# Kernel optimization log

Hardware: AMD Instinct MI355X
Metric: run time of the kernel (lower is better)

The kernel has to match this reference:

```python
import jax, jax.numpy as jnp
import numpy as np

N_NODES = 100000   # batch of target nodes
K = 10             # sampled neighbors per node (num_sample default)
VOCAB = 200000     # total graph nodes in embedding table
D = 128            # embed_dim


def setup_inputs() -> dict:
    key = jax.random.key(0)
    k1, k2, k3 = jax.random.split(key, 3)
    embed_table = jax.random.normal(k1, (VOCAB, D), dtype=jnp.float32)
    attn_w = jax.random.normal(k2, (D,), dtype=jnp.float32)
    neigh_idx = jax.random.randint(k3, (N_NODES, K), 0, VOCAB, dtype=jnp.int64)
    return {"embed_table": embed_table, "attn_w": attn_w, "neigh_idx": neigh_idx}


def reference(embed_table, attn_w, neigh_idx):
    # Gather neighbor embeddings: [N, K, D] (the irregular-access hot spot)
    feats = embed_table[neigh_idx]
    # attention_fc: Linear(D, 1, bias=False) -> scores [N, K]
    scores = jnp.einsum("nkd,d->nk", feats, attn_w)
    # softmax over the neighbor axis (dim=0 in the per-node torch loop == K here)
    weights = jax.nn.softmax(scores, axis=1)
    # attention-weighted sum of neighbor features -> [N, D]
    out = jnp.einsum("nk,nkd->nd", weights, feats)
    return out
```

## Files before the change

### kernel.cpp

```cpp
#include <hip/hip_runtime.h>
#include <math.h>


#define KNEIGH 10
#define DIM 128

__global__ __launch_bounds__(256) void attn_agg_kernel(
    const float* __restrict__ table,
    const float* __restrict__ attn_w,
    const int*   __restrict__ idx,
    float*       __restrict__ out,
    int n_nodes)
{
    const int gtid = blockIdx.x * blockDim.x + threadIdx.x;
    const int node = gtid >> 6;
    const int lane = threadIdx.x & 63;
    if (node >= n_nodes) return;

    const float2 wv = *(const float2*)(attn_w + lane * 2);

    int my_idx = 0;
    if (lane < KNEIGH) my_idx = idx[node * KNEIGH + lane];

    float2 f[KNEIGH];
    float  s[KNEIGH];

    #pragma unroll
    for (int k = 0; k < KNEIGH; ++k) {
        const int id = __shfl(my_idx, k, 64);
        f[k] = *(const float2*)(table + (size_t)id * DIM + lane * 2);
        float p = f[k].x * wv.x + f[k].y * wv.y;
        #pragma unroll
        for (int off = 32; off >= 1; off >>= 1)
            p += __shfl_xor(p, off, 64);
        s[k] = p;
    }

    float m = s[0];
    #pragma unroll
    for (int k = 1; k < KNEIGH; ++k) m = fmaxf(m, s[k]);
    float denom = 0.f;
    #pragma unroll
    for (int k = 0; k < KNEIGH; ++k) { s[k] = __expf(s[k] - m); denom += s[k]; }
    const float inv = 1.0f / denom;

    float2 acc = make_float2(0.f, 0.f);
    #pragma unroll
    for (int k = 0; k < KNEIGH; ++k) {
        const float wk = s[k] * inv;
        acc.x = fmaf(wk, f[k].x, acc.x);
        acc.y = fmaf(wk, f[k].y, acc.y);
    }

    *(float2*)(out + (size_t)node * DIM + lane * 2) = acc;
}

extern "C" void kernel_launch(void* const* d_in, const int* in_sizes, int n_in,
                              void* d_out, int out_size, void* d_ws, size_t ws_size,
                              hipStream_t stream) {
    const float* table  = (const float*)d_in[0];
    const float* attn_w = (const float*)d_in[1];
    const int*   idx    = (const int*)d_in[2];
    float*       out    = (float*)d_out;

    const int n_nodes = in_sizes[2] / KNEIGH;
    const int waves_per_block = 4;
    const int blocks = (n_nodes + waves_per_block - 1) / waves_per_block;
    attn_agg_kernel<<<blocks, 256, 0, stream>>>(table, attn_w, idx, out, n_nodes);
}
```

Measured before the change: 209.5 us.

## Split wave into two halves each gathering alternate neighbors with float4 loads

Result: no change. 209.5 us (+0.0%).

```diff
diff --git a/kernel.cpp b/kernel.cpp
--- a/kernel.cpp
+++ b/kernel.cpp
@@ -3,7 +3,8 @@
 
 
 #define KNEIGH 10
-#define DIM 128
+#define NPAIR  5
+#define DIM    128
 
 __global__ __launch_bounds__(256) void attn_agg_kernel(
     const float* __restrict__ table,
@@ -14,26 +15,36 @@
 {
     const int gtid = blockIdx.x * blockDim.x + threadIdx.x;
     const int node = gtid >> 6;
+    if (node >= n_nodes) return;
     const int lane = threadIdx.x & 63;
-    if (node >= n_nodes) return;
+    const int half = lane >> 5;
+    const int sub  = lane & 31;
 
-    const float2 wv = *(const float2*)(attn_w + lane * 2);
+    const float4 w4 = *(const float4*)(attn_w + sub * 4);
 
     int my_idx = 0;
     if (lane < KNEIGH) my_idx = idx[node * KNEIGH + lane];
 
-    float2 f[KNEIGH];
-    float  s[KNEIGH];
+    int id[NPAIR];
+    #pragma unroll
+    for (int j = 0; j < NPAIR; ++j)
+        id[j] = __shfl(my_idx, 2 * j + half, 64);
 
+    float4 f[NPAIR];
     #pragma unroll
-    for (int k = 0; k < KNEIGH; ++k) {
-        const int id = __shfl(my_idx, k, 64);
-        f[k] = *(const float2*)(table + (size_t)id * DIM + lane * 2);
-        float p = f[k].x * wv.x + f[k].y * wv.y;
+    for (int j = 0; j < NPAIR; ++j)
+        f[j] = *(const float4*)(table + (size_t)id[j] * DIM + sub * 4);
+
+    float s[KNEIGH];
+    #pragma unroll
+    for (int j = 0; j < NPAIR; ++j) {
+        float p = f[j].x * w4.x + f[j].y * w4.y + f[j].z * w4.z + f[j].w * w4.w;
         #pragma unroll
-        for (int off = 32; off >= 1; off >>= 1)
+        for (int off = 16; off >= 1; off >>= 1)
             p += __shfl_xor(p, off, 64);
-        s[k] = p;
+        const float q = __shfl_xor(p, 32, 64);
+        s[2 * j]     = half ? q : p;
+        s[2 * j + 1] = half ? p : q;
     }
 
     float m = s[0];
@@ -44,15 +55,23 @@
     for (int k = 0; k < KNEIGH; ++k) { s[k] = __expf(s[k] - m); denom += s[k]; }
     const float inv = 1.0f / denom;
 
-    float2 acc = make_float2(0.f, 0.f);
+    float4 acc = make_float4(0.f, 0.f, 0.f, 0.f);
     #pragma unroll
-    for (int k = 0; k < KNEIGH; ++k) {
-        const float wk = s[k] * inv;
-        acc.x = fmaf(wk, f[k].x, acc.x);
-        acc.y = fmaf(wk, f[k].y, acc.y);
+    for (int j = 0; j < NPAIR; ++j) {
+        const float wk = (half ? s[2 * j + 1] : s[2 * j]) * inv;
+        acc.x = fmaf(wk, f[j].x, acc.x);
+        acc.y = fmaf(wk, f[j].y, acc.y);
+        acc.z = fmaf(wk, f[j].z, acc.z);
+        acc.w = fmaf(wk, f[j].w, acc.w);
     }
 
-    *(float2*)(out + (size_t)node * DIM + lane * 2) = acc;
+    acc.x += __shfl_xor(acc.x, 32, 64);
+    acc.y += __shfl_xor(acc.y, 32, 64);
+    acc.z += __shfl_xor(acc.z, 32, 64);
+    acc.w += __shfl_xor(acc.w, 32, 64);
+
+    if (half == 0)
+        *(float4*)(out + (size_t)node * DIM + sub * 4) = acc;
 }
 
 extern "C" void kernel_launch(void* const* d_in, const int* in_sizes, int n_in,
```

## Precompute per-row scores and bf16 table, then gather half-width rows

Applied to the files above, without the earlier changes.

New measurement: 219.7 us. 4.9% more time.

```diff
diff --git a/kernel.cpp b/kernel.cpp
--- a/kernel.cpp
+++ b/kernel.cpp
@@ -3,9 +3,114 @@
 
 
 #define KNEIGH 10
-#define DIM 128
+#define NPAIR  5
+#define DIM    128
 
-__global__ __launch_bounds__(256) void attn_agg_kernel(
+__global__ __launch_bounds__(256) void convert_score_kernel(
+    const float*  __restrict__ table,
+    const float*  __restrict__ attn_w,
+    unsigned int* __restrict__ bf_table,
+    float*        __restrict__ scores,
+    int vocab)
+{
+    const int gtid = blockIdx.x * blockDim.x + threadIdx.x;
+    const int row  = gtid >> 6;
+    if (row >= vocab) return;
+    const int lane = threadIdx.x & 63;
+
+    const float2 f = *(const float2*)(table  + (size_t)row * DIM + lane * 2);
+    const float2 w = *(const float2*)(attn_w + lane * 2);
+
+    float p = f.x * w.x + f.y * w.y;
+    #pragma unroll
+    for (int off = 32; off >= 1; off >>= 1)
+        p += __shfl_xor(p, off, 64);
+
+    unsigned int bx = __float_as_uint(f.x);
+    unsigned int by = __float_as_uint(f.y);
+    bx = (bx + 0x7fffu + ((bx >> 16) & 1u)) >> 16;
+    by = (by + 0x7fffu + ((by >> 16) & 1u)) & 0xffff0000u;
+    bf_table[(size_t)row * 64 + lane] = bx | by;
+
+    if (lane == 0) scores[row] = p;
+}
+
+__global__ __launch_bounds__(256) void attn_gather_kernel(
+    const unsigned int* __restrict__ bf_table,
+    const float*        __restrict__ scores,
+    const int*          __restrict__ idx,
+    float*              __restrict__ out,
+    int n_nodes)
+{
+    const int gtid = blockIdx.x * blockDim.x + threadIdx.x;
+    const int node = gtid >> 6;
+    if (node >= n_nodes) return;
+    const int lane = threadIdx.x & 63;
+    const int half = lane >> 5;
+    const int sub  = lane & 31;
+
+    const int base = __builtin_amdgcn_readfirstlane(node) * KNEIGH;
+    int id0 = idx[base + 0], id1 = idx[base + 1], id2 = idx[base + 2],
+        id3 = idx[base + 3], id4 = idx[base + 4], id5 = idx[base + 5],
+        id6 = idx[base + 6], id7 = idx[base + 7], id8 = idx[base + 8],
+        id9 = idx[base + 9];
+    float s0 = scores[id0], s1 = scores[id1], s2 = scores[id2],
+          s3 = scores[id3], s4 = scores[id4], s5 = scores[id5],
+          s6 = scores[id6], s7 = scores[id7], s8 = scores[id8],
+          s9 = scores[id9];
+
+    const int r0 = half ? id1 : id0;
+    const int r1 = half ? id3 : id2;
+    const int r2 = half ? id5 : id4;
+    const int r3 = half ? id7 : id6;
+    const int r4 = half ? id9 : id8;
+
+    uint2 g0 = *(const uint2*)(bf_table + (size_t)r0 * 64 + sub * 2);
+    uint2 g1 = *(const uint2*)(bf_table + (size_t)r1 * 64 + sub * 2);
+    uint2 g2 = *(const uint2*)(bf_table + (size_t)r2 * 64 + sub * 2);
+    uint2 g3 = *(const uint2*)(bf_table + (size_t)r3 * 64 + sub * 2);
+    uint2 g4 = *(const uint2*)(bf_table + (size_t)r4 * 64 + sub * 2);
+
+    float m = fmaxf(fmaxf(fmaxf(fmaxf(s0, s1), fmaxf(s2, s3)),
+                          fmaxf(fmaxf(s4, s5), fmaxf(s6, s7))),
+                    fmaxf(s8, s9));
+    s0 = __expf(s0 - m); s1 = __expf(s1 - m); s2 = __expf(s2 - m);
+    s3 = __expf(s3 - m); s4 = __expf(s4 - m); s5 = __expf(s5 - m);
+    s6 = __expf(s6 - m); s7 = __expf(s7 - m); s8 = __expf(s8 - m);
+    s9 = __expf(s9 - m);
+    const float inv = 1.0f /
+        (s0 + s1 + s2 + s3 + s4 + s5 + s6 + s7 + s8 + s9);
+    const float w0 = (half ? s1 : s0) * inv;
+    const float w1 = (half ? s3 : s2) * inv;
+    const float w2 = (half ? s5 : s4) * inv;
+    const float w3 = (half ? s7 : s6) * inv;
+    const float w4 = (half ? s9 : s8) * inv;
+
+    float4 acc = make_float4(0.f, 0.f, 0.f, 0.f);
+    #define ACCUM(G, WK)                                                   \
+        {                                                                  \
+            const float e0 = __uint_as_float((G).x << 16);                 \
+            const float e1 = __uint_as_float((G).x & 0xffff0000u);         \
+            const float e2 = __uint_as_float((G).y << 16);                 \
+            const float e3 = __uint_as_float((G).y & 0xffff0000u);         \
+            acc.x = fmaf((WK), e0, acc.x);                                 \
+            acc.y = fmaf((WK), e1, acc.y);                                 \
+            acc.z = fmaf((WK), e2, acc.z);                                 \
+            acc.w = fmaf((WK), e3, acc.w);                                 \
+        }
+    ACCUM(g0, w0) ACCUM(g1, w1) ACCUM(g2, w2) ACCUM(g3, w3) ACCUM(g4, w4)
+    #undef ACCUM
+
+    acc.x += __shfl_xor(acc.x, 32, 64);
+    acc.y += __shfl_xor(acc.y, 32, 64);
+    acc.z += __shfl_xor(acc.z, 32, 64);
+    acc.w += __shfl_xor(acc.w, 32, 64);
+
+    if (half == 0)
+        *(float4*)(out + (size_t)node * DIM + sub * 4) = acc;
+}
+
+__global__ __launch_bounds__(256) void attn_agg_fp32_kernel(
     const float* __restrict__ table,
     const float* __restrict__ attn_w,
     const int*   __restrict__ idx,
@@ -18,13 +123,11 @@
     if (node >= n_nodes) return;
 
     const float2 wv = *(const float2*)(attn_w + lane * 2);
-
     int my_idx = 0;
     if (lane < KNEIGH) my_idx = idx[node * KNEIGH + lane];
 
     float2 f[KNEIGH];
     float  s[KNEIGH];
-
     #pragma unroll
     for (int k = 0; k < KNEIGH; ++k) {
         const int id = __shfl(my_idx, k, 64);
@@ -35,7 +138,6 @@
             p += __shfl_xor(p, off, 64);
         s[k] = p;
     }
-
     float m = s[0];
     #pragma unroll
     for (int k = 1; k < KNEIGH; ++k) m = fmaxf(m, s[k]);
@@ -43,7 +145,6 @@
     #pragma unroll
     for (int k = 0; k < KNEIGH; ++k) { s[k] = __expf(s[k] - m); denom += s[k]; }
     const float inv = 1.0f / denom;
-
     float2 acc = make_float2(0.f, 0.f);
     #pragma unroll
     for (int k = 0; k < KNEIGH; ++k) {
@@ -51,7 +152,6 @@
         acc.x = fmaf(wk, f[k].x, acc.x);
         acc.y = fmaf(wk, f[k].y, acc.y);
     }
-
     *(float2*)(out + (size_t)node * DIM + lane * 2) = acc;
 }
 
@@ -63,8 +163,26 @@
     const int*   idx    = (const int*)d_in[2];
     float*       out    = (float*)d_out;
 
+    const int vocab   = in_sizes[0] / DIM;
     const int n_nodes = in_sizes[2] / KNEIGH;
-    const int waves_per_block = 4;
-    const int blocks = (n_nodes + waves_per_block - 1) / waves_per_block;
-    attn_agg_kernel<<<blocks, 256, 0, stream>>>(table, attn_w, idx, out, n_nodes);
+
+    const size_t bf_bytes = (size_t)vocab * (DIM / 2) * sizeof(unsigned int);
+    const size_t need     = bf_bytes + (size_t)vocab * sizeof(float);
+
+    if (ws_size >= need) {
+        unsigned int* bf_table = (unsigned int*)d_ws;
+        float*        scores   = (float*)((char*)d_ws + bf_bytes);
+
+        const int blocks1 = (vocab + 3) / 4;
+        convert_score_kernel<<<blocks1, 256, 0, stream>>>(
+            table, attn_w, bf_table, scores, vocab);
+
+        const int blocks2 = (n_nodes + 3) / 4;
+        attn_gather_kernel<<<blocks2, 256, 0, stream>>>(
+            bf_table, scores, idx, out, n_nodes);
+    } else {
+        const int blocks = (n_nodes + 3) / 4;
+        attn_agg_fp32_kernel<<<blocks, 256, 0, stream>>>(
+            table, attn_w, idx, out, n_nodes);
+    }
 }
```

## Precompute per-row scores and bf16 table copy, then gather half-width rows

Applied to the files above, without the earlier changes.

New measurement: 208.3 us. Within noise of the previous version (-0.6%).

```diff
diff --git a/kernel.cpp b/kernel.cpp
--- a/kernel.cpp
+++ b/kernel.cpp
@@ -3,9 +3,164 @@
 
 
 #define KNEIGH 10
-#define DIM 128
-
-__global__ __launch_bounds__(256) void attn_agg_kernel(
+#define DIM    128
+
+__global__ __launch_bounds__(256) void convert_score_kernel(
+    const float*  __restrict__ table,
+    const float*  __restrict__ attn_w,
+    unsigned int* __restrict__ bf_table,
+    float*        __restrict__ scores,
+    int vocab)
+{
+    const int gtid = blockIdx.x * blockDim.x + threadIdx.x;
+    const int lane = threadIdx.x & 63;
+    const int half = lane >> 5;
+    const int sub  = lane & 31;
+    const int row  = (gtid >> 6) * 2 + half;
+    if (row >= vocab) return;
+
+    const float4 f  = *(const float4*)(table + (size_t)row * DIM + sub * 4);
+    const float4 w4 = *(const float4*)(attn_w + sub * 4);
+
+    float p = f.x * w4.x + f.y * w4.y + f.z * w4.z + f.w * w4.w;
+    #pragma unroll
+    for (int off = 16; off >= 1; off >>= 1)
+        p += __shfl_xor(p, off, 64);
+
+    unsigned int ux = __float_as_uint(f.x), uy = __float_as_uint(f.y);
+    unsigned int uz = __float_as_uint(f.z), uw = __float_as_uint(f.w);
+    ux = (ux + 0x7fffu + ((ux >> 16) & 1u)) >> 16;
+    uy = (uy + 0x7fffu + ((uy >> 16) & 1u)) & 0xffff0000u;
+    uz = (uz + 0x7fffu + ((uz >> 16) & 1u)) >> 16;
+    uw = (uw + 0x7fffu + ((uw >> 16) & 1u)) & 0xffff0000u;
+    uint2 packed = make_uint2(ux | uy, uz | uw);
+    *(uint2*)(bf_table + (size_t)row * 64 + sub * 2) = packed;
+
+    if (sub == 0) scores[row] = p;
+}
+
+__global__ __launch_bounds__(256) void attn_gather_kernel(
+    const unsigned int* __restrict__ bf_table,
+    const float*        __restrict__ scores,
+    const int*          __restrict__ idx,
+    float*              __restrict__ out,
+    int n_nodes)
+{
+    const int gtid = blockIdx.x * blockDim.x + threadIdx.x;
+    const int wid  = gtid >> 6;
+    const int n0   = wid * 2;
+    if (n0 >= n_nodes) return;
+    const int  n1   = n0 + 1;
+    const bool has1 = (n1 < n_nodes);
+    const int  lane = threadIdx.x & 63;
+    const int  q    = lane >> 4;
+    const int  sub  = lane & 15;
+
+    const int b0 = __builtin_amdgcn_readfirstlane(n0) * KNEIGH;
+    const int b1 = has1 ? b0 + KNEIGH : b0;
+
+    const int ia0 = idx[b0+0], ia1 = idx[b0+1], ia2 = idx[b0+2], ia3 = idx[b0+3],
+              ia4 = idx[b0+4], ia5 = idx[b0+5], ia6 = idx[b0+6], ia7 = idx[b0+7],
+              ia8 = idx[b0+8], ia9 = idx[b0+9];
+    const int ib0 = idx[b1+0], ib1 = idx[b1+1], ib2 = idx[b1+2], ib3 = idx[b1+3],
+              ib4 = idx[b1+4], ib5 = idx[b1+5], ib6 = idx[b1+6], ib7 = idx[b1+7],
+              ib8 = idx[b1+8], ib9 = idx[b1+9];
+
+    const int r0 = (q == 0) ? ia0 : (q == 1) ? ia1 : (q == 2) ? ia2 : ia3;
+    const int r1 = (q == 0) ? ia4 : (q == 1) ? ia5 : (q == 2) ? ia6 : ia7;
+    const int r2 = (q == 0) ? ia8 : (q == 1) ? ia9 : (q == 2) ? ib0 : ib1;
+    const int r3 = (q == 0) ? ib2 : (q == 1) ? ib3 : (q == 2) ? ib4 : ib5;
+    const int r4 = (q == 0) ? ib6 : (q == 1) ? ib7 : (q == 2) ? ib8 : ib9;
+
+    const uint4 g0 = *(const uint4*)(bf_table + (size_t)r0 * 64 + sub * 4);
+    const uint4 g1 = *(const uint4*)(bf_table + (size_t)r1 * 64 + sub * 4);
+    const uint4 g2 = *(const uint4*)(bf_table + (size_t)r2 * 64 + sub * 4);
+    const uint4 g3 = *(const uint4*)(bf_table + (size_t)r3 * 64 + sub * 4);
+    const uint4 g4 = *(const uint4*)(bf_table + (size_t)r4 * 64 + sub * 4);
+
+    float sa0 = scores[ia0], sa1 = scores[ia1], sa2 = scores[ia2],
+          sa3 = scores[ia3], sa4 = scores[ia4], sa5 = scores[ia5],
+          sa6 = scores[ia6], sa7 = scores[ia7], sa8 = scores[ia8],
+          sa9 = scores[ia9];
+    float sb0 = scores[ib0], sb1 = scores[ib1], sb2 = scores[ib2],
+          sb3 = scores[ib3], sb4 = scores[ib4], sb5 = scores[ib5],
+          sb6 = scores[ib6], sb7 = scores[ib7], sb8 = scores[ib8],
+          sb9 = scores[ib9];
+
+    float ma = fmaxf(fmaxf(fmaxf(fmaxf(sa0, sa1), fmaxf(sa2, sa3)),
+                           fmaxf(fmaxf(sa4, sa5), fmaxf(sa6, sa7))),
+                     fmaxf(sa8, sa9));
+    sa0 = __expf(sa0 - ma); sa1 = __expf(sa1 - ma); sa2 = __expf(sa2 - ma);
+    sa3 = __expf(sa3 - ma); sa4 = __expf(sa4 - ma); sa5 = __expf(sa5 - ma);
+    sa6 = __expf(sa6 - ma); sa7 = __expf(sa7 - ma); sa8 = __expf(sa8 - ma);
+    sa9 = __expf(sa9 - ma);
+    const float inva = 1.0f /
+        (sa0 + sa1 + sa2 + sa3 + sa4 + sa5 + sa6 + sa7 + sa8 + sa9);
+
+    float mb = fmaxf(fmaxf(fmaxf(fmaxf(sb0, sb1), fmaxf(sb2, sb3)),
+                           fmaxf(fmaxf(sb4, sb5), fmaxf(sb6, sb7))),
+                     fmaxf(sb8, sb9));
+    sb0 = __expf(sb0 - mb); sb1 = __expf(sb1 - mb); sb2 = __expf(sb2 - mb);
+    sb3 = __expf(sb3 - mb); sb4 = __expf(sb4 - mb); sb5 = __expf(sb5 - mb);
+    sb6 = __expf(sb6 - mb); sb7 = __expf(sb7 - mb); sb8 = __expf(sb8 - mb);
+    sb9 = __expf(sb9 - mb);
+    const float invb = 1.0f /
+        (sb0 + sb1 + sb2 + sb3 + sb4 + sb5 + sb6 + sb7 + sb8 + sb9);
+
+    const float w0 = ((q == 0) ? sa0 : (q == 1) ? sa1 : (q == 2) ? sa2 : sa3) * inva;
+    const float w1 = ((q == 0) ? sa4 : (q == 1) ? sa5 : (q == 2) ? sa6 : sa7) * inva;
+    const float w2 = (q == 0) ? sa8 * inva : (q == 1) ? sa9 * inva
+                   : (q == 2) ? sb0 * invb : sb1 * invb;
+    const float w3 = ((q == 0) ? sb2 : (q == 1) ? sb3 : (q == 2) ? sb4 : sb5) * invb;
+    const float w4 = ((q == 0) ? sb6 : (q == 1) ? sb7 : (q == 2) ? sb8 : sb9) * invb;
+
+    float a0=0.f,a1=0.f,a2=0.f,a3=0.f,a4=0.f,a5=0.f,a6=0.f,a7=0.f;
+    float b0f=0.f,b1f=0.f,b2f=0.f,b3f=0.f,b4f=0.f,b5f=0.f,b6f=0.f,b7f=0.f;
+
+    #define UNPK(G, W, A0,A1,A2,A3,A4,A5,A6,A7)                                \
+        A0 = fmaf((W), __uint_as_float((G).x << 16),          A0);             \
+        A1 = fmaf((W), __uint_as_float((G).x & 0xffff0000u),  A1);             \
+        A2 = fmaf((W), __uint_as_float((G).y << 16),          A2);             \
+        A3 = fmaf((W), __uint_as_float((G).y & 0xffff0000u),  A3);             \
+        A4 = fmaf((W), __uint_as_float((G).z << 16),          A4);             \
+        A5 = fmaf((W), __uint_as_float((G).z & 0xffff0000u),  A5);             \
+        A6 = fmaf((W), __uint_as_float((G).w << 16),          A6);             \
+        A7 = fmaf((W), __uint_as_float((G).w & 0xffff0000u),  A7);
+
+    UNPK(g0, w0, a0,a1,a2,a3,a4,a5,a6,a7)
+    UNPK(g1, w1, a0,a1,a2,a3,a4,a5,a6,a7)
+    {
+        float c0=0.f,c1=0.f,c2=0.f,c3=0.f,c4=0.f,c5=0.f,c6=0.f,c7=0.f;
+        UNPK(g2, w2, c0,c1,c2,c3,c4,c5,c6,c7)
+        const bool lo = (q < 2);
+        a0 += lo ? c0 : 0.f; a1 += lo ? c1 : 0.f; a2 += lo ? c2 : 0.f;
+        a3 += lo ? c3 : 0.f; a4 += lo ? c4 : 0.f; a5 += lo ? c5 : 0.f;
+        a6 += lo ? c6 : 0.f; a7 += lo ? c7 : 0.f;
+        b0f += lo ? 0.f : c0; b1f += lo ? 0.f : c1; b2f += lo ? 0.f : c2;
+        b3f += lo ? 0.f : c3; b4f += lo ? 0.f : c4; b5f += lo ? 0.f : c5;
+        b6f += lo ? 0.f : c6; b7f += lo ? 0.f : c7;
+    }
+    UNPK(g3, w3, b0f,b1f,b2f,b3f,b4f,b5f,b6f,b7f)
+    UNPK(g4, w4, b0f,b1f,b2f,b3f,b4f,b5f,b6f,b7f)
+    #undef UNPK
+
+    #define RED(X) X += __shfl_xor(X, 16, 64); X += __shfl_xor(X, 32, 64);
+    RED(a0) RED(a1) RED(a2) RED(a3) RED(a4) RED(a5) RED(a6) RED(a7)
+    RED(b0f) RED(b1f) RED(b2f) RED(b3f) RED(b4f) RED(b5f) RED(b6f) RED(b7f)
+    #undef RED
+
+    if (q == 0) {
+        float* p = out + (size_t)n0 * DIM + sub * 8;
+        *(float4*)(p)     = make_float4(a0, a1, a2, a3);
+        *(float4*)(p + 4) = make_float4(a4, a5, a6, a7);
+    } else if (q == 1 && has1) {
+        float* p = out + (size_t)n1 * DIM + sub * 8;
+        *(float4*)(p)     = make_float4(b0f, b1f, b2f, b3f);
+        *(float4*)(p + 4) = make_float4(b4f, b5f, b6f, b7f);
+    }
+}
+
+__global__ __launch_bounds__(256) void attn_agg_fp32_kernel(
     const float* __restrict__ table,
     const float* __restrict__ attn_w,
     const int*   __restrict__ idx,
@@ -18,13 +173,11 @@
     if (node >= n_nodes) return;
 
     const float2 wv = *(const float2*)(attn_w + lane * 2);
-
     int my_idx = 0;
     if (lane < KNEIGH) my_idx = idx[node * KNEIGH + lane];
 
     float2 f[KNEIGH];
     float  s[KNEIGH];
-
     #pragma unroll
     for (int k = 0; k < KNEIGH; ++k) {
         const int id = __shfl(my_idx, k, 64);
@@ -35,7 +188,6 @@
             p += __shfl_xor(p, off, 64);
         s[k] = p;
     }
-
     float m = s[0];
     #pragma unroll
     for (int k = 1; k < KNEIGH; ++k) m = fmaxf(m, s[k]);
@@ -43,7 +195,6 @@
     #pragma unroll
     for (int k = 0; k < KNEIGH; ++k) { s[k] = __expf(s[k] - m); denom += s[k]; }
     const float inv = 1.0f / denom;
-
     float2 acc = make_float2(0.f, 0.f);
     #pragma unroll
     for (int k = 0; k < KNEIGH; ++k) {
@@ -51,7 +202,6 @@
         acc.x = fmaf(wk, f[k].x, acc.x);
         acc.y = fmaf(wk, f[k].y, acc.y);
     }
-
     *(float2*)(out + (size_t)node * DIM + lane * 2) = acc;
 }
 
@@ -63,8 +213,28 @@
     const int*   idx    = (const int*)d_in[2];
     float*       out    = (float*)d_out;
 
+    const int vocab   = in_sizes[0] / DIM;
     const int n_nodes = in_sizes[2] / KNEIGH;
-    const int waves_per_block = 4;
-    const int blocks = (n_nodes + waves_per_block - 1) / waves_per_block;
-    attn_agg_kernel<<<blocks, 256, 0, stream>>>(table, attn_w, idx, out, n_nodes);
-}
+
+    const size_t bf_bytes = (size_t)vocab * (DIM / 2) * sizeof(unsigned int);
+    const size_t need     = bf_bytes + (size_t)vocab * sizeof(float);
+
+    if (ws_size >= need) {
+        unsigned int* bf_table = (unsigned int*)d_ws;
+        float*        scores   = (float*)((char*)d_ws + bf_bytes);
+
+        const int waves1  = (vocab + 1) / 2;
+        const int blocks1 = (waves1 + 3) / 4;
+        convert_score_kernel<<<blocks1, 256, 0, stream>>>(
+            table, attn_w, bf_table, scores, vocab);
+
+        const int waves2  = (n_nodes + 1) / 2;
+        const int blocks2 = (waves2 + 3) / 4;
+        attn_gather_kernel<<<blocks2, 256, 0, stream>>>(
+            bf_table, scores, idx, out, n_nodes);
+    } else {
+        const int blocks = (n_nodes + 3) / 4;
+        attn_agg_fp32_kernel<<<blocks, 256, 0, stream>>>(
+            table, attn_w, idx, out, n_nodes);
+    }
+}
```
